# Kernel optimization log

Measured on AMD Instinct MI355X. Metric: run time of the kernel, lower is better.

## Reference

```python
import jax, jax.numpy as jnp
import numpy as np

EPS = 1e-05
RFN = 0.5  # blend factor between group-norm path and per-token layer-norm path


def _ln_last(x, eps):
    # layer_norm over last dim, no affine (matches F.layer_norm(x, x.shape[-1:]))
    mu = jnp.mean(x, axis=-1, keepdims=True)
    var = jnp.mean(jnp.square(x - mu), axis=-1, keepdims=True)
    return (x - mu) * jax.lax.rsqrt(var + eps)


def setup_inputs() -> dict:
    key = jax.random.key(0)
    kx, kw, kb = jax.random.split(key, 3)
    B, T, D, G = 8, 4000, 1024, 5
    x = jax.random.normal(kx, (B, T, D), dtype=jnp.float32)
    mask = jnp.ones((G, T // G), dtype=jnp.int32)  # default dense mask: 5 contiguous groups
    weight = jax.random.normal(kw, (D,), dtype=jnp.float32)
    bias = jax.random.normal(kb, (D,), dtype=jnp.float32)
    return {"x": x, "mask": mask, "weight": weight, "bias": bias}


def reference(x, mask, weight, bias):
    B, T, D = x.shape
    G = mask.shape[0]          # number of groups from mask rows
    L = T // G                 # tokens per group (dense ones mask => contiguous blocks)

    # rfn_mode == 'in': per-token layer norm over feature dim
    lned = _ln_last(x, EPS)

    # per-group layer norm over (group_tokens, features) jointly, matching
    # F.layer_norm(x[:, i], normalized_shape=x[:, i].shape[-2:])
    xg = x.reshape(B, G, L, D)
    mu = jnp.mean(xg, axis=(-2, -1), keepdims=True)
    var = jnp.mean(jnp.square(xg - mu), axis=(-2, -1), keepdims=True)
    gn = ((xg - mu) * jax.lax.rsqrt(var + EPS)).reshape(B, T, D)

    return (RFN * gn + (1.0 - RFN) * lned) * weight + bias
```

## Files before the change

### kernel.cpp

```cpp
#include <hip/hip_runtime.h>


#define EPS 1e-5f
#define NUM_G 5

__global__ __launch_bounds__(256) void stats_kernel(
    const float4* __restrict__ x, float2* __restrict__ tstats) {
  const int wave = threadIdx.x >> 6, lane = threadIdx.x & 63;
  const int row0 = blockIdx.x * 8 + wave * 2;
  const long b0 = (long)row0 * 256;

  float4 a[4], b[4];
  #pragma unroll
  for (int j = 0; j < 4; ++j) a[j] = x[b0 + lane + 64 * j];
  #pragma unroll
  for (int j = 0; j < 4; ++j) b[j] = x[b0 + 256 + lane + 64 * j];

  float s0 = 0.f, q0 = 0.f, s1 = 0.f, q1 = 0.f;
  #pragma unroll
  for (int j = 0; j < 4; ++j) {
    s0 += (a[j].x + a[j].y) + (a[j].z + a[j].w);
    q0 += (a[j].x * a[j].x + a[j].y * a[j].y) + (a[j].z * a[j].z + a[j].w * a[j].w);
    s1 += (b[j].x + b[j].y) + (b[j].z + b[j].w);
    q1 += (b[j].x * b[j].x + b[j].y * b[j].y) + (b[j].z * b[j].z + b[j].w * b[j].w);
  }
  #pragma unroll
  for (int off = 1; off < 64; off <<= 1) {
    s0 += __shfl_xor(s0, off, 64);  q0 += __shfl_xor(q0, off, 64);
    s1 += __shfl_xor(s1, off, 64);  q1 += __shfl_xor(q1, off, 64);
  }
  if (lane == 0) {
    float2 st0; st0.x = s0; st0.y = q0;
    float2 st1; st1.x = s1; st1.y = q1;
    tstats[row0]     = st0;
    tstats[row0 + 1] = st1;
  }
}

__global__ __launch_bounds__(256) void greduce_kernel(
    const float2* __restrict__ tstats, float2* __restrict__ gstats,
    int L, float invNg) {
  const int g = blockIdx.x;
  float s = 0.f, sq = 0.f;
  for (int j = threadIdx.x; j < L; j += 256) {
    float2 st = tstats[(long)g * L + j];
    s += st.x; sq += st.y;
  }
  #pragma unroll
  for (int off = 1; off < 64; off <<= 1) {
    s  += __shfl_xor(s,  off, 64);
    sq += __shfl_xor(sq, off, 64);
  }
  __shared__ float ls[4], lq[4];
  const int wave = threadIdx.x >> 6, lane = threadIdx.x & 63;
  if (lane == 0) { ls[wave] = s; lq[wave] = sq; }
  __syncthreads();
  if (threadIdx.x == 0) {
    const float S  = (ls[0] + ls[1]) + (ls[2] + ls[3]);
    const float SQ = (lq[0] + lq[1]) + (lq[2] + lq[3]);
    const float gmu = S * invNg;
    float2 o;
    o.x = gmu;
    o.y = rsqrtf(SQ * invNg - gmu * gmu + EPS) * 0.5f;
    gstats[g] = o;
  }
}

__global__ __launch_bounds__(256) void out_kernel(
    const float4* __restrict__ x, const float2* __restrict__ gstats,
    const float2* __restrict__ tstats,
    const float4* __restrict__ weight, const float4* __restrict__ bias,
    float4* __restrict__ out, int L, float invD) {
  const int tid = threadIdx.x;
  const float4 w  = weight[tid];
  const float4 bb = bias[tid];
  const int row0 = blockIdx.x * 4;

  #pragma unroll
  for (int r = 0; r < 4; ++r) {
    const int row = row0 + r;
    const float2 gst = gstats[row / L];
    const float gmu = gst.x, grs = gst.y;
    const float2 st = tstats[row];
    const float tmu = st.x * invD;
    const float trs = rsqrtf(st.y * invD - tmu * tmu + EPS) * 0.5f;

    const long base = (long)row * 256;
    const float4 v = x[base + tid];
    float4 o;
    o.x = ((v.x - gmu) * grs + (v.x - tmu) * trs) * w.x + bb.x;
    o.y = ((v.y - gmu) * grs + (v.y - tmu) * trs) * w.y + bb.y;
    o.z = ((v.z - gmu) * grs + (v.z - tmu) * trs) * w.z + bb.z;
    o.w = ((v.w - gmu) * grs + (v.w - tmu) * trs) * w.w + bb.w;
    out[base + tid] = o;
  }
}

extern "C" void kernel_launch(void* const* d_in, const int* in_sizes, int n_in,
                              void* d_out, int out_size, void* d_ws, size_t ws_size,
                              hipStream_t stream) {
  const float* x      = (const float*)d_in[0];
  const float* weight = (const float*)d_in[2];
  const float* bias   = (const float*)d_in[3];
  float* out          = (float*)d_out;

  const int D = in_sizes[2];
  const int T = in_sizes[1];
  const int B = in_sizes[0] / (T * D);
  const int L = T / NUM_G;
  const int n_rows = B * T;
  const long Ng = (long)L * D;

  float2* tstats = (float2*)d_ws;
  float2* gstats = (float2*)((char*)d_ws + (size_t)n_rows * sizeof(float2));

  dim3 blk(256);
  stats_kernel<<<dim3(n_rows / 8), blk, 0, stream>>>((const float4*)x, tstats);

  greduce_kernel<<<dim3(B * NUM_G), blk, 0, stream>>>(
      tstats, gstats, L, 1.0f / (float)Ng);

  out_kernel<<<dim3(n_rows / 4), blk, 0, stream>>>(
      (const float4*)x, gstats, tstats,
      (const float4*)weight, (const float4*)bias,
      (float4*)out, L, 1.0f / D);
}
```

Baseline: 251.7 us.

## Fold group reduction into stats and output kernels, dropping greduce launch

The stats kernel now also writes one partial group sum and sum of squares per block. The separate group-reduce kernel is removed, and each output block re-reduces its group's 100 partials before normalizing, now covering 8 rows per block instead of 4. This saves one kernel launch and the serialized, low-occupancy reduce step that ran on only 40 blocks. In exchange, every output block does redundant partial reads and an extra barrier, and it relies on L being divisible by 8.

```diff
diff --git a/kernel.cpp b/kernel.cpp
--- a/kernel.cpp
+++ b/kernel.cpp
@@ -5,7 +5,8 @@
 #define NUM_G 5
 
 __global__ __launch_bounds__(256) void stats_kernel(
-    const float4* __restrict__ x, float2* __restrict__ tstats) {
+    const float4* __restrict__ x, float2* __restrict__ tstats,
+    float2* __restrict__ gpart) {
   const int wave = threadIdx.x >> 6, lane = threadIdx.x & 63;
   const int row0 = blockIdx.x * 8 + wave * 2;
   const long b0 = (long)row0 * 256;
@@ -29,58 +30,64 @@
     s0 += __shfl_xor(s0, off, 64);  q0 += __shfl_xor(q0, off, 64);
     s1 += __shfl_xor(s1, off, 64);  q1 += __shfl_xor(q1, off, 64);
   }
+
+  __shared__ float ls[4], lq[4];
   if (lane == 0) {
     float2 st0; st0.x = s0; st0.y = q0;
     float2 st1; st1.x = s1; st1.y = q1;
     tstats[row0]     = st0;
     tstats[row0 + 1] = st1;
+    ls[wave] = s0 + s1;
+    lq[wave] = q0 + q1;
   }
-}
-
-__global__ __launch_bounds__(256) void greduce_kernel(
-    const float2* __restrict__ tstats, float2* __restrict__ gstats,
-    int L, float invNg) {
-  const int g = blockIdx.x;
-  float s = 0.f, sq = 0.f;
-  for (int j = threadIdx.x; j < L; j += 256) {
-    float2 st = tstats[(long)g * L + j];
-    s += st.x; sq += st.y;
-  }
-  #pragma unroll
-  for (int off = 1; off < 64; off <<= 1) {
-    s  += __shfl_xor(s,  off, 64);
-    sq += __shfl_xor(sq, off, 64);
-  }
-  __shared__ float ls[4], lq[4];
-  const int wave = threadIdx.x >> 6, lane = threadIdx.x & 63;
-  if (lane == 0) { ls[wave] = s; lq[wave] = sq; }
   __syncthreads();
   if (threadIdx.x == 0) {
-    const float S  = (ls[0] + ls[1]) + (ls[2] + ls[3]);
-    const float SQ = (lq[0] + lq[1]) + (lq[2] + lq[3]);
-    const float gmu = S * invNg;
-    float2 o;
-    o.x = gmu;
-    o.y = rsqrtf(SQ * invNg - gmu * gmu + EPS) * 0.5f;
-    gstats[g] = o;
+    float2 p;
+    p.x = (ls[0] + ls[1]) + (ls[2] + ls[3]);
+    p.y = (lq[0] + lq[1]) + (lq[2] + lq[3]);
+    gpart[blockIdx.x] = p;
   }
 }
 
 __global__ __launch_bounds__(256) void out_kernel(
-    const float4* __restrict__ x, const float2* __restrict__ gstats,
-    const float2* __restrict__ tstats,
+    const float4* __restrict__ x, const float2* __restrict__ tstats,
+    const float2* __restrict__ gpart,
     const float4* __restrict__ weight, const float4* __restrict__ bias,
-    float4* __restrict__ out, int L, float invD) {
+    float4* __restrict__ out, int ppg, int bpg, float invNg, float invD) {
   const int tid = threadIdx.x;
+  const int wave = tid >> 6, lane = tid & 63;
+  const int g = blockIdx.x / bpg;
+
+  float s = 0.f, q = 0.f;
+  for (int j = tid; j < ppg; j += 256) {
+    float2 p = gpart[g * ppg + j];
+    s += p.x; q += p.y;
+  }
+  #pragma unroll
+  for (int off = 1; off < 64; off <<= 1) {
+    s += __shfl_xor(s, off, 64);
+    q += __shfl_xor(q, off, 64);
+  }
+  __shared__ float ls[4], lq[4], sg[2];
+  if (lane == 0) { ls[wave] = s; lq[wave] = q; }
+  __syncthreads();
+  if (tid == 0) {
+    const float S  = (ls[0] + ls[1]) + (ls[2] + ls[3]);
+    const float SQ = (lq[0] + lq[1]) + (lq[2] + lq[3]);
+    const float gmu = S * invNg;
+    sg[0] = gmu;
+    sg[1] = rsqrtf(SQ * invNg - gmu * gmu + EPS) * 0.5f;
+  }
+  __syncthreads();
+  const float gmu = sg[0], grs = sg[1];
+
   const float4 w  = weight[tid];
   const float4 bb = bias[tid];
-  const int row0 = blockIdx.x * 4;
+  const int row0 = blockIdx.x * 8;
 
   #pragma unroll
-  for (int r = 0; r < 4; ++r) {
+  for (int r = 0; r < 8; ++r) {
     const int row = row0 + r;
-    const float2 gst = gstats[row / L];
-    const float gmu = gst.x, grs = gst.y;
     const float2 st = tstats[row];
     const float tmu = st.x * invD;
     const float trs = rsqrtf(st.y * invD - tmu * tmu + EPS) * 0.5f;
@@ -112,16 +119,17 @@
   const long Ng = (long)L * D;
 
   float2* tstats = (float2*)d_ws;
-  float2* gstats = (float2*)((char*)d_ws + (size_t)n_rows * sizeof(float2));
+  float2* gpart  = (float2*)((char*)d_ws + (size_t)n_rows * sizeof(float2));
+
+  const int ppg = L / 8;
+  const int bpg = L / 8;
 
   dim3 blk(256);
-  stats_kernel<<<dim3(n_rows / 8), blk, 0, stream>>>((const float4*)x, tstats);
+  stats_kernel<<<dim3(n_rows / 8), blk, 0, stream>>>(
+      (const float4*)x, tstats, gpart);
 
-  greduce_kernel<<<dim3(B * NUM_G), blk, 0, stream>>>(
-      tstats, gstats, L, 1.0f / (float)Ng);
-
-  out_kernel<<<dim3(n_rows / 4), blk, 0, stream>>>(
-      (const float4*)x, gstats, tstats,
+  out_kernel<<<dim3(n_rows / 8), blk, 0, stream>>>(
+      (const float4*)x, tstats, gpart,
       (const float4*)weight, (const float4*)bias,
-      (float4*)out, L, 1.0f / D);
+      (float4*)out, ppg, bpg, 1.0f / (float)Ng, 1.0f / D);
 }
```

Result: no change. 248.3 us (-1.3%).
